# Performance work log

Hardware: AMD Instinct MI355X
Metric: run time of the kernel (lower is better)

Reference implementation:

```python
import jax, jax.numpy as jnp
import numpy as np

B, S, D, H, HD = 2, 2048, 1024, 16, 64
DFF = 4 * D
EPS = 1e-6


def _rms(x, w):
    return w * (x * jax.lax.rsqrt(jnp.mean(x * x, axis=-1, keepdims=True) + EPS))


def _rope(x, rope):
    # x: [B, H, S, HD], rope: [S, HD, 2]
    cos = rope[..., 0][None, None]
    sin = rope[..., 1][None, None]
    xr = x.reshape(*x.shape[:-1], -1, 2)
    rot = jnp.stack([-xr[..., 1], xr[..., 0]], axis=-1).reshape(x.shape)
    return x * cos + rot * sin


def setup_inputs() -> dict:
    key = jax.random.key(0)
    ks = jax.random.split(key, 10)
    w = lambda k, shape: jax.random.normal(k, shape, jnp.float32) * 0.02
    return {
        "hidden_states": jax.random.normal(ks[0], (B, S, D), jnp.float32),
        "timestep": jax.random.normal(ks[1], (B, D), jnp.float32),
        "rope_pos_embed": jax.random.normal(ks[2], (S, HD, 2), jnp.float32),
        "adaln_w": w(ks[3], (6 * D, D)),
        "adaln_b": jnp.zeros((6 * D,), jnp.float32),
        "wq": w(ks[4], (D, D)),
        "wk": w(ks[5], (D, D)),
        "wv": w(ks[6], (D, D)),
        "wo": w(ks[7], (D, D)),
        "q_norm_w": jnp.ones((D,), jnp.float32),
        "k_norm_w": jnp.ones((D,), jnp.float32),
        "norm3_w": jnp.ones((D,), jnp.float32),
        "fc1_w": w(ks[8], (DFF, D)),
        "fc1_b": jnp.zeros((DFF,), jnp.float32),
        "fc2_w": w(ks[9], (D, DFF)),
        "fc2_b": jnp.zeros((D,), jnp.float32),
    }


def reference(hidden_states, timestep, rope_pos_embed, adaln_w, adaln_b,
              wq, wk, wv, wo, q_norm_w, k_norm_w, norm3_w,
              fc1_w, fc1_b, fc2_w, fc2_b):
    x = hidden_states  # [B, S, D]
    # AdaLayerNorm: emb = Linear(SiLU(timestep)) -> 6 modulation chunks, broadcast over seq
    emb = jax.nn.silu(timestep) @ adaln_w.T + adaln_b  # [B, 6D]
    sh_msa, sc_msa, g_msa, sh_mlp, sc_mlp, g_mlp = jnp.split(emb[:, None, :], 6, axis=-1)
    mu = jnp.mean(x, axis=-1, keepdims=True)
    var = jnp.mean((x - mu) ** 2, axis=-1, keepdims=True)
    ln = (x - mu) * jax.lax.rsqrt(var + EPS)
    xm = ln * (1.0 + sc_msa) + sh_msa  # modulated input to attention

    # Attention: projections + RMSNorm over inner_dim + RoPE + SDPA
    q = _rms(xm @ wq.T, q_norm_w)
    k = _rms(xm @ wk.T, k_norm_w)
    v = xm @ wv.T
    q = q.reshape(B, S, H, HD).transpose(0, 2, 1, 3)
    k = k.reshape(B, S, H, HD).transpose(0, 2, 1, 3)
    v = v.reshape(B, S, H, HD).transpose(0, 2, 1, 3)
    q = _rope(q, rope_pos_embed)
    k = _rope(k, rope_pos_embed)
    scores = jnp.einsum('bhqd,bhkd->bhqk', q, k) * (HD ** -0.5)
    attn = jax.nn.softmax(scores, axis=-1)
    o = jnp.einsum('bhqk,bhkd->bhqd', attn, v)
    o = o.transpose(0, 2, 1, 3).reshape(B, S, H * HD) @ wo.T

    h = x + g_msa * o  # gated residual

    # MLP branch with AdaLN scale/shift on RMSNorm output
    n3 = _rms(h, norm3_w)
    nm = n3 * (1.0 + sc_mlp) + sh_mlp
    ff = jax.nn.gelu(nm @ fc1_w.T + fc1_b, approximate=True) @ fc2_w.T + fc2_b
    return h + g_mlp * ff
```

## Files before the change

### kernel.cpp

```cpp
#include <hip/hip_runtime.h>
#include <cstdint>
#include <cstddef>

typedef unsigned short ushort_t;
typedef __attribute__((ext_vector_type(8))) short s8v;
typedef __attribute__((ext_vector_type(4))) short s4v;
typedef __attribute__((ext_vector_type(4))) float f4v;

#define MFMA16(a, b, c) __builtin_amdgcn_mfma_f32_16x16x32_bf16(a, b, c, 0, 0, 0)

__device__ __forceinline__ ushort_t f2bf(float f) {
  union { float f; unsigned u; } a; a.f = f;
  return (ushort_t)((a.u + 0x7fffu + ((a.u >> 16) & 1u)) >> 16);
}
__device__ __forceinline__ float bf2f(ushort_t h) {
  union { unsigned u; float f; } a; a.u = ((unsigned)h) << 16; return a.f;
}

__device__ __forceinline__ void gload16(const void* g, void* l) {
  __builtin_amdgcn_global_load_lds(
      (__attribute__((address_space(1))) void*)(uintptr_t)g,
      (__attribute__((address_space(3))) void*)(unsigned)(uintptr_t)l,
      16, 0, 0);
}

__launch_bounds__(256)
__global__ void convert_w(const float* __restrict__ wq, const float* __restrict__ wk,
                          const float* __restrict__ wv, const float* __restrict__ wo,
                          const float* __restrict__ f1, const float* __restrict__ f2,
                          ushort_t* __restrict__ dqkv, ushort_t* __restrict__ dwo,
                          ushort_t* __restrict__ df1, ushort_t* __restrict__ df2)
{
  const int blk = blockIdx.x;
  const float* src; ushort_t* dst; int off;
  if      (blk < 1024) { src = wq; dst = dqkv;            off = blk; }
  else if (blk < 2048) { src = wk; dst = dqkv + 1048576;  off = blk - 1024; }
  else if (blk < 3072) { src = wv; dst = dqkv + 2097152;  off = blk - 2048; }
  else if (blk < 4096) { src = wo; dst = dwo;             off = blk - 3072; }
  else if (blk < 8192) { src = f1; dst = df1;             off = blk - 4096; }
  else                 { src = f2; dst = df2;             off = blk - 8192; }
  const int idx = off * 1024 + threadIdx.x * 4;
  float4 v = *(const float4*)(src + idx);
  s4v o;
  o[0] = (short)f2bf(v.x); o[1] = (short)f2bf(v.y);
  o[2] = (short)f2bf(v.z); o[3] = (short)f2bf(v.w);
  *(s4v*)(dst + idx) = o;
}

__launch_bounds__(256)
__global__ void adaln(const float* __restrict__ ts, const float* __restrict__ w,
                      const float* __restrict__ bias, float* __restrict__ emb)
{
  const int j = blockIdx.x * 4 + (threadIdx.x >> 6);
  const int lane = threadIdx.x & 63;
  const float* wr = w + (size_t)j * 1024;
  float s0 = 0.f, s1 = 0.f;
  for (int i = lane; i < 1024; i += 64) {
    const float wv = wr[i];
    const float t0 = ts[i], t1 = ts[1024 + i];
    s0 += wv * (t0 / (1.f + __expf(-t0)));
    s1 += wv * (t1 / (1.f + __expf(-t1)));
  }
  #pragma unroll
  for (int m = 32; m; m >>= 1) { s0 += __shfl_down(s0, m); s1 += __shfl_down(s1, m); }
  if (!lane) { emb[j] = s0 + bias[j]; emb[6144 + j] = s1 + bias[j]; }
}

__launch_bounds__(256)
__global__ void ln_mod(const float* __restrict__ x, const float* __restrict__ emb,
                       ushort_t* __restrict__ xm)
{
  const int row = blockIdx.x, b = row >> 11, tid = threadIdx.x;
  const float* xr = x + (size_t)row * 1024;
  const int c = tid * 4;
  float4 v = *(const float4*)(xr + c);
  float s  = v.x + v.y + v.z + v.w;
  float s2 = v.x*v.x + v.y*v.y + v.z*v.z + v.w*v.w;
  #pragma unroll
  for (int m = 32; m; m >>= 1) { s += __shfl_down(s, m); s2 += __shfl_down(s2, m); }
  __shared__ float red[8];
  const int wave = tid >> 6, lane = tid & 63;
  if (!lane) { red[wave] = s; red[4 + wave] = s2; }
  __syncthreads();
  const float mu = (red[0] + red[1] + red[2] + red[3]) * (1.f / 1024.f);
  const float ms = (red[4] + red[5] + red[6] + red[7]) * (1.f / 1024.f);
  const float rstd = rsqrtf(ms - mu * mu + 1e-6f);
  const float* sh = emb + b * 6144;
  const float* sc = emb + b * 6144 + 1024;
  float4 shv = *(const float4*)(sh + c);
  float4 scv = *(const float4*)(sc + c);
  s4v ov;
  ov[0] = (short)f2bf((v.x - mu) * rstd * (1.f + scv.x) + shv.x);
  ov[1] = (short)f2bf((v.y - mu) * rstd * (1.f + scv.y) + shv.y);
  ov[2] = (short)f2bf((v.z - mu) * rstd * (1.f + scv.z) + shv.z);
  ov[3] = (short)f2bf((v.w - mu) * rstd * (1.f + scv.w) + shv.w);
  *(s4v*)(xm + (size_t)row * 1024 + c) = ov;
}

template<int EPI, int TN>
__launch_bounds__(256)
__global__ void gemm_bt(const ushort_t* __restrict__ A, const ushort_t* __restrict__ Bw,
                        int K, int N,
                        ushort_t* __restrict__ outb, float* __restrict__ outf,
                        const float* __restrict__ bias, const float* __restrict__ resid,
                        const float* __restrict__ emb, int gate_off)
{
  constexpr int JN = TN / 32;
  constexpr int BUFB = TN * 32;
  __shared__ ushort_t As[2 * 128 * 32];
  __shared__ ushort_t Bs[2 * BUFB];
  const int tid = threadIdx.x;
  const int wave = tid >> 6, lane = tid & 63;
  const int quad = lane >> 4, r = lane & 15;
  const int m0 = blockIdx.y * 128, n0 = blockIdx.x * TN;
  const int wm = (wave >> 1) * 64, wn = (wave & 1) * (TN / 2);

  const int srow = wave * 16 + (lane >> 2);
  const int scol = (lane & 3) * 8;
  const ushort_t* ag = A  + (size_t)(m0 + srow) * K + scol;
  const ushort_t* bg = Bw + (size_t)(n0 + srow) * K + scol;
  const size_t rowK64 = (size_t)64 * K;

  f4v acc[4][JN] = {};

  {
    ushort_t* as = As + wave * 512;
    ushort_t* bs = Bs + wave * 512;
    gload16(ag,          as);
    gload16(ag + rowK64, as + 2048);
    gload16(bg,          bs);
    if (TN == 128) gload16(bg + rowK64, bs + 2048);
    ag += 32; bg += 32;
  }

  const int nIter = K >> 5;
  int cur = 0;
  for (int it = 0; it < nIter - 1; it++) {
    __syncthreads();
    {
      ushort_t* as = As + (cur ^ 1) * 4096 + wave * 512;
      ushort_t* bs = Bs + (cur ^ 1) * BUFB + wave * 512;
      gload16(ag,          as);
      gload16(ag + rowK64, as + 2048);
      gload16(bg,          bs);
      if (TN == 128) gload16(bg + rowK64, bs + 2048);
      ag += 32; bg += 32;
    }
    const ushort_t* ab = As + cur * 4096;
    const ushort_t* bb = Bs + cur * BUFB;
    s8v af[4], bf[JN];
    #pragma unroll
    for (int i = 0; i < 4; i++)
      af[i] = *(const s8v*)(ab + (wm + i * 16 + r) * 32 + quad * 8);
    #pragma unroll
    for (int j = 0; j < JN; j++)
      bf[j] = *(const s8v*)(bb + (wn + j * 16 + r) * 32 + quad * 8);
    #pragma unroll
    for (int i = 0; i < 4; i++)
      #pragma unroll
      for (int j = 0; j < JN; j++)
        acc[i][j] = MFMA16(af[i], bf[j], acc[i][j]);
    cur ^= 1;
  }
  __syncthreads();
  {
    const ushort_t* ab = As + cur * 4096;
    const ushort_t* bb = Bs + cur * BUFB;
    s8v af[4], bf[JN];
    #pragma unroll
    for (int i = 0; i < 4; i++)
      af[i] = *(const s8v*)(ab + (wm + i * 16 + r) * 32 + quad * 8);
    #pragma unroll
    for (int j = 0; j < JN; j++)
      bf[j] = *(const s8v*)(bb + (wn + j * 16 + r) * 32 + quad * 8);
    #pragma unroll
    for (int i = 0; i < 4; i++)
      #pragma unroll
      for (int j = 0; j < JN; j++)
        acc[i][j] = MFMA16(af[i], bf[j], acc[i][j]);
  }

  #pragma unroll
  for (int i = 0; i < 4; i++) {
    const int row = m0 + wm + i * 16 + quad * 4;
    #pragma unroll
    for (int j = 0; j < JN; j++) {
      const int col = n0 + wn + j * 16 + r;
      #pragma unroll
      for (int rr = 0; rr < 4; rr++) {
        float v = acc[i][j][rr];
        const int rw = row + rr;
        const size_t idx = (size_t)rw * N + col;
        if (EPI == 0) {
          outb[idx] = f2bf(v);
        } else if (EPI == 1) {
          const int b = rw >> 11;
          outf[idx] = resid[idx] + emb[b * 6144 + gate_off + col] * v;
        } else if (EPI == 2) {
          v += bias[col];
          const float u = 0.7978845608028654f * (v + 0.044715f * v * v * v);
          const float e = __expf(2.f * u);
          const float th = 1.f - 2.f / (e + 1.f);
          outb[idx] = f2bf(0.5f * v * (1.f + th));
        } else {
          const int b = rw >> 11;
          outf[idx] = resid[idx] + emb[b * 6144 + gate_off + col] * (v + bias[col]);
        }
      }
    }
  }
}

__launch_bounds__(256)
__global__ void qkv_post(const ushort_t* __restrict__ qkv, const float* __restrict__ rope,
                         const float* __restrict__ qw, const float* __restrict__ kw,
                         ushort_t* __restrict__ q_r, ushort_t* __restrict__ k_r,
                         ushort_t* __restrict__ v_r)
{
  const int row = blockIdx.x, b = row >> 11, s = row & 2047, tid = threadIdx.x;
  const ushort_t* base = qkv + (size_t)row * 3072;
  const int c = tid * 4;
  s4v qv = *(const s4v*)(base + c);
  s4v kv = *(const s4v*)(base + 1024 + c);
  s4v vv = *(const s4v*)(base + 2048 + c);
  float qf[4], kf[4]; float sq = 0.f, sk = 0.f;
  #pragma unroll
  for (int i = 0; i < 4; i++) {
    qf[i] = bf2f((ushort_t)qv[i]); kf[i] = bf2f((ushort_t)kv[i]);
    sq += qf[i] * qf[i]; sk += kf[i] * kf[i];
  }
  #pragma unroll
  for (int m = 32; m; m >>= 1) { sq += __shfl_down(sq, m); sk += __shfl_down(sk, m); }
  __shared__ float red[8];
  const int wave = tid >> 6, lane = tid & 63;
  if (!lane) { red[wave] = sq; red[4 + wave] = sk; }
  __syncthreads();
  const float rq = rsqrtf((red[0]+red[1]+red[2]+red[3]) * (1.f/1024.f) + 1e-6f)
                   * 0.18033688011112042f;
  const float rk = rsqrtf((red[4]+red[5]+red[6]+red[7]) * (1.f/1024.f) + 1e-6f);

  const int h = c >> 6, d = c & 63;
  const float* rp = rope + ((size_t)s * 64 + d) * 2;
  float4 r01 = *(const float4*)(rp);
  float4 r23 = *(const float4*)(rp + 4);
  const float q0 = qf[0]*rq*qw[c], q1 = qf[1]*rq*qw[c+1];
  const float q2 = qf[2]*rq*qw[c+2], q3 = qf[3]*rq*qw[c+3];
  const float k0 = kf[0]*rk*kw[c], k1 = kf[1]*rk*kw[c+1];
  const float k2 = kf[2]*rk*kw[c+2], k3 = kf[3]*rk*kw[c+3];
  s4v qo, ko;
  qo[0] = (short)f2bf(q0 * r01.x - q1 * r01.y);
  qo[1] = (short)f2bf(q1 * r01.z + q0 * r01.w);
  qo[2] = (short)f2bf(q2 * r23.x - q3 * r23.y);
  qo[3] = (short)f2bf(q3 * r23.z + q2 * r23.w);
  ko[0] = (short)f2bf(k0 * r01.x - k1 * r01.y);
  ko[1] = (short)f2bf(k1 * r01.z + k0 * r01.w);
  ko[2] = (short)f2bf(k2 * r23.x - k3 * r23.y);
  ko[3] = (short)f2bf(k3 * r23.z + k2 * r23.w);
  const size_t rowbase = ((size_t)(b * 16 + h) * 2048 + s) * 64;
  const int d_s = (((d >> 3) ^ (s & 7)) << 3) | (d & 7);
  *(s4v*)(q_r + rowbase + d) = qo;
  *(s4v*)(k_r + rowbase + d_s) = ko;
  *(s4v*)(v_r + rowbase + d) = vv;
}

__launch_bounds__(256)
__global__ void vtrans(const ushort_t* __restrict__ v_r, ushort_t* __restrict__ v_t)
{
  const int bh = blockIdx.x >> 5, st = blockIdx.x & 31;
  const int s0 = st * 64;
  __shared__ ushort_t tile[64 * 72];
  const int tid = threadIdx.x;
  #pragma unroll
  for (int rep = 0; rep < 2; rep++) {
    const int idx = rep * 256 + tid;
    const int sr = idx >> 3, dc = (idx & 7) << 3;
    s8v val = *(const s8v*)(v_r + ((size_t)bh * 2048 + s0 + sr) * 64 + dc);
    *(s8v*)(tile + sr * 72 + dc) = val;
  }
  __syncthreads();
  #pragma unroll
  for (int rep = 0; rep < 2; rep++) {
    const int idx = rep * 256 + tid;
    const int d = idx >> 3;
    const int scs = (((idx & 7) ^ (d & 7)) << 3);
    s8v val;
    const int sc = (idx & 7) << 3;
    #pragma unroll
    for (int j = 0; j < 8; j++) val[j] = (short)tile[(sc + j) * 72 + d];
    *(s8v*)(v_t + ((size_t)bh * 64 + d) * 2048 + s0 + scs) = val;
  }
}

__launch_bounds__(256)
__global__ void flash(const ushort_t* __restrict__ q_r, const ushort_t* __restrict__ k_r,
                      const ushort_t* __restrict__ v_t, ushort_t* __restrict__ attn)
{
  __shared__ ushort_t Ksh[64 * 64];
  __shared__ ushort_t Vsh[64 * 64];
  __shared__ ushort_t Psh[4][16 * 64];
  const int bh = blockIdx.x >> 5, qb = blockIdx.x & 31;
  const int tid = threadIdx.x, wave = tid >> 6, lane = tid & 63;
  const int quad = lane >> 4, r = lane & 15;
  const int rx = r & 7;
  const int q0 = qb * 64 + wave * 16;
  const size_t bhS = (size_t)bh * 2048;

  s8v aq0 = *(const s8v*)(q_r + (bhS + q0 + r) * 64 + quad * 8);
  s8v aq1 = *(const s8v*)(q_r + (bhS + q0 + r) * 64 + 32 + quad * 8);

  f4v o[4] = {};
  float mi = -1e30f, li = 0.f;

  const ushort_t* kg = k_r + bhS * 64 + wave * 1024 + lane * 8;
  const ushort_t* vg0 = v_t + ((size_t)bh * 64 + wave * 16 + (lane >> 3)) * 2048
                        + (lane & 7) * 8;
  const ushort_t* vg1 = vg0 + (size_t)8 * 2048;
  ushort_t* kl0 = Ksh + wave * 1024;
  ushort_t* kl1 = Ksh + wave * 1024 + 512;
  ushort_t* vl0 = Vsh + wave * 1024;
  ushort_t* vl1 = Vsh + wave * 1024 + 512;
  ushort_t* pw = &Psh[wave][0];

  for (int kb = 0; kb < 2048; kb += 64) {
    __syncthreads();
    gload16(kg,        kl0);
    gload16(kg + 512,  kl1);
    gload16(vg0 + kb,  vl0);
    gload16(vg1 + kb,  vl1);
    kg += 64 * 64;
    __syncthreads();

    f4v st[4];
    #pragma unroll
    for (int t = 0; t < 4; t++) {
      const ushort_t* krow = Ksh + (t * 16 + r) * 64;
      s8v k0 = *(const s8v*)(krow + (((quad) ^ rx) << 3));
      s8v k1 = *(const s8v*)(krow + (((4 + quad) ^ rx) << 3));
      f4v z = {};
      z = MFMA16(k0, aq0, z);
      z = MFMA16(k1, aq1, z);
      st[t] = z;
    }

    float mloc = st[0][0];
    #pragma unroll
    for (int t = 0; t < 4; t++)
      #pragma unroll
      for (int rr = 0; rr < 4; rr++) mloc = fmaxf(mloc, st[t][rr]);
    mloc = fmaxf(mloc, __shfl_xor(mloc, 16));
    mloc = fmaxf(mloc, __shfl_xor(mloc, 32));
    const float mn = fmaxf(mi, mloc);
    const float al = exp2f(mi - mn);
    float ls = 0.f;
    float p[4][4];
    #pragma unroll
    for (int t = 0; t < 4; t++)
      #pragma unroll
      for (int rr = 0; rr < 4; rr++) {
        p[t][rr] = exp2f(st[t][rr] - mn);
        ls += p[t][rr];
      }
    ls += __shfl_xor(ls, 16);
    ls += __shfl_xor(ls, 32);
    li = al * li + ls;
    mi = mn;

    #pragma unroll
    for (int t = 0; t < 4; t++) {
      s4v pb;
      pb[0] = (short)f2bf(p[t][0]); pb[1] = (short)f2bf(p[t][1]);
      pb[2] = (short)f2bf(p[t][2]); pb[3] = (short)f2bf(p[t][3]);
      const int idx = r * 64 + (((((t << 1) | (quad >> 1))) ^ rx) << 3) + (quad & 1) * 4;
      *(s4v*)(pw + idx) = pb;
    }

    float alo[4];
    #pragma unroll
    for (int rr = 0; rr < 4; rr++) alo[rr] = __shfl(al, quad * 4 + rr);
    #pragma unroll
    for (int nt = 0; nt < 4; nt++)
      #pragma unroll
      for (int rr = 0; rr < 4; rr++) o[nt][rr] *= alo[rr];

    asm volatile("s_waitcnt lgkmcnt(0)" ::: "memory");

    #pragma unroll
    for (int kc = 0; kc < 2; kc++) {
      s8v ap = *(const s8v*)(pw + r * 64 + ((((kc << 2) | quad) ^ rx) << 3));
      #pragma unroll
      for (int nt = 0; nt < 4; nt++) {
        s8v bv = *(const s8v*)(Vsh + (nt * 16 + r) * 64 + ((((kc << 2) | quad) ^ rx) << 3));
        o[nt] = MFMA16(ap, bv, o[nt]);
      }
    }
  }

  const int h = bh & 15, b = bh >> 4;
  const float linv = 1.f / li;
  #pragma unroll
  for (int rr = 0; rr < 4; rr++) {
    const float inv = __shfl(linv, quad * 4 + rr);
    const size_t orow = ((size_t)(b * 2048 + q0 + quad * 4 + rr)) * 1024 + h * 64;
    #pragma unroll
    for (int nt = 0; nt < 4; nt++)
      attn[orow + nt * 16 + r] = f2bf(o[nt][rr] * inv);
  }
}

__launch_bounds__(256)
__global__ void rms3_mod(const float* __restrict__ h, const float* __restrict__ emb,
                         const float* __restrict__ w3, ushort_t* __restrict__ nm)
{
  const int row = blockIdx.x, b = row >> 11, tid = threadIdx.x;
  const float* hr = h + (size_t)row * 1024;
  const int c = tid * 4;
  float4 v = *(const float4*)(hr + c);
  float s2 = v.x*v.x + v.y*v.y + v.z*v.z + v.w*v.w;
  #pragma unroll
  for (int m = 32; m; m >>= 1) s2 += __shfl_down(s2, m);
  __shared__ float red[4];
  const int wave = tid >> 6, lane = tid & 63;
  if (!lane) red[wave] = s2;
  __syncthreads();
  const float rms = rsqrtf((red[0] + red[1] + red[2] + red[3]) * (1.f / 1024.f) + 1e-6f);
  const float* sh = emb + b * 6144 + 3072;
  const float* sc = emb + b * 6144 + 4096;
  float4 shv = *(const float4*)(sh + c);
  float4 scv = *(const float4*)(sc + c);
  float4 wv  = *(const float4*)(w3 + c);
  s4v ov;
  ov[0] = (short)f2bf(v.x * rms * wv.x * (1.f + scv.x) + shv.x);
  ov[1] = (short)f2bf(v.y * rms * wv.y * (1.f + scv.y) + shv.y);
  ov[2] = (short)f2bf(v.z * rms * wv.z * (1.f + scv.z) + shv.z);
  ov[3] = (short)f2bf(v.w * rms * wv.w * (1.f + scv.w) + shv.w);
  *(s4v*)(nm + (size_t)row * 1024 + c) = ov;
}

extern "C" void kernel_launch(void* const* d_in, const int* in_sizes, int n_in,
                              void* d_out, int out_size, void* d_ws, size_t ws_size,
                              hipStream_t stream)
{
  const float* x    = (const float*)d_in[0];
  const float* ts   = (const float*)d_in[1];
  const float* rope = (const float*)d_in[2];
  const float* adw  = (const float*)d_in[3];
  const float* adb  = (const float*)d_in[4];
  const float* wq   = (const float*)d_in[5];
  const float* wk   = (const float*)d_in[6];
  const float* wv   = (const float*)d_in[7];
  const float* wo   = (const float*)d_in[8];
  const float* qnw  = (const float*)d_in[9];
  const float* knw  = (const float*)d_in[10];
  const float* n3w  = (const float*)d_in[11];
  const float* f1w  = (const float*)d_in[12];
  const float* f1b  = (const float*)d_in[13];
  const float* f2w  = (const float*)d_in[14];
  const float* f2b  = (const float*)d_in[15];

  char* ws = (char*)d_ws;
  ushort_t* WQKV = (ushort_t*)(ws + 0);
  ushort_t* WO   = (ushort_t*)(ws + 6291456);
  ushort_t* F1   = (ushort_t*)(ws + 8388608);
  ushort_t* F2   = (ushort_t*)(ws + 16777216);
  float*    EMB  = (float*)   (ws + 25165824);
  float*    H    = (float*)   (ws + 25214976);
  ushort_t* XM   = (ushort_t*)(ws + 41992192);
  ushort_t* QKV  = (ushort_t*)(ws + 50380800);
  ushort_t* QR   = (ushort_t*)(ws + 75546624);
  ushort_t* KR   = (ushort_t*)(ws + 83935232);
  ushort_t* VR   = (ushort_t*)(ws + 92323840);
  ushort_t* VT   = (ushort_t*)(ws + 100712448);
  ushort_t* ATTN = XM;
  ushort_t* NM   = QKV;
  ushort_t* FF1  = QR;

  convert_w<<<12288, 256, 0, stream>>>(wq, wk, wv, wo, f1w, f2w, WQKV, WO, F1, F2);
  adaln<<<1536, 256, 0, stream>>>(ts, adw, adb, EMB);
  ln_mod<<<4096, 256, 0, stream>>>(x, EMB, XM);
  gemm_bt<0, 128><<<dim3(24, 32), 256, 0, stream>>>(XM, WQKV, 1024, 3072,
      QKV, nullptr, nullptr, nullptr, nullptr, 0);
  qkv_post<<<4096, 256, 0, stream>>>(QKV, rope, qnw, knw, QR, KR, VR);
  vtrans<<<1024, 256, 0, stream>>>(VR, VT);
  flash<<<1024, 256, 0, stream>>>(QR, KR, VT, ATTN);
  gemm_bt<1, 64><<<dim3(16, 32), 256, 0, stream>>>(ATTN, WO, 1024, 1024,
      nullptr, H, nullptr, x, EMB, 2048);
  rms3_mod<<<4096, 256, 0, stream>>>(H, EMB, n3w, NM);
  gemm_bt<2, 128><<<dim3(32, 32), 256, 0, stream>>>(NM, F1, 1024, 4096,
      FF1, nullptr, f1b, nullptr, nullptr, 0);
  gemm_bt<3, 64><<<dim3(16, 32), 256, 0, stream>>>(FF1, F2, 4096, 1024,
      nullptr, (float*)d_out, f2b, H, EMB, 5120);
}
```

Before: 441.9 us.

## Double flash attention KV tile to 128 and use fast exp2 and packed bf16 rounding

The flash kernel now processes 128 keys per iteration instead of 64, which halves the number of barrier pairs and online-softmax rescales per key. It also swaps exp2f for the hardware exp2 builtin and packs bf16 P values with a simple rounding add plus byte-perm instead of round-to-nearest-even. The trade-off is double the shared memory and more registers per wave (eight score tiles), which can lower occupancy. The bf16 rounding changes slightly from ties-to-even to round-half-up.

```diff
diff --git a/kernel.cpp b/kernel.cpp
--- a/kernel.cpp
+++ b/kernel.cpp
@@ -15,6 +15,9 @@
 }
 __device__ __forceinline__ float bf2f(ushort_t h) {
   union { unsigned u; float f; } a; a.u = ((unsigned)h) << 16; return a.f;
+}
+__device__ __forceinline__ unsigned fbits(float f) {
+  union { float f; unsigned u; } a; a.f = f; return a.u;
 }
 
 __device__ __forceinline__ void gload16(const void* g, void* l) {
@@ -295,9 +298,9 @@
 __global__ void flash(const ushort_t* __restrict__ q_r, const ushort_t* __restrict__ k_r,
                       const ushort_t* __restrict__ v_t, ushort_t* __restrict__ attn)
 {
-  __shared__ ushort_t Ksh[64 * 64];
-  __shared__ ushort_t Vsh[64 * 64];
-  __shared__ ushort_t Psh[4][16 * 64];
+  __shared__ ushort_t Ksh[128 * 64];
+  __shared__ ushort_t Vsh[64 * 128];
+  __shared__ ushort_t Psh[4][16 * 128];
   const int bh = blockIdx.x >> 5, qb = blockIdx.x & 31;
   const int tid = threadIdx.x, wave = tid >> 6, lane = tid & 63;
   const int quad = lane >> 4, r = lane & 15;
@@ -311,30 +314,27 @@
   f4v o[4] = {};
   float mi = -1e30f, li = 0.f;
 
-  const ushort_t* kg = k_r + bhS * 64 + wave * 1024 + lane * 8;
-  const ushort_t* vg0 = v_t + ((size_t)bh * 64 + wave * 16 + (lane >> 3)) * 2048
-                        + (lane & 7) * 8;
-  const ushort_t* vg1 = vg0 + (size_t)8 * 2048;
-  ushort_t* kl0 = Ksh + wave * 1024;
-  ushort_t* kl1 = Ksh + wave * 1024 + 512;
-  ushort_t* vl0 = Vsh + wave * 1024;
-  ushort_t* vl1 = Vsh + wave * 1024 + 512;
+  const ushort_t* kg = k_r + (bhS + wave * 32 + (lane >> 3)) * 64 + (lane & 7) * 8;
+  ushort_t* kl = Ksh + wave * 2048 + lane * 8;
+  const ushort_t* vg = v_t + ((size_t)bh * 64 + wave * 16 + (lane >> 4)) * 2048
+                       + (lane & 15) * 8;
+  ushort_t* vl = Vsh + (wave * 16 + (lane >> 4)) * 128 + (lane & 15) * 8;
   ushort_t* pw = &Psh[wave][0];
 
-  for (int kb = 0; kb < 2048; kb += 64) {
+  for (int kb = 0; kb < 2048; kb += 128) {
     __syncthreads();
-    gload16(kg,        kl0);
-    gload16(kg + 512,  kl1);
-    gload16(vg0 + kb,  vl0);
-    gload16(vg1 + kb,  vl1);
-    kg += 64 * 64;
+    #pragma unroll
+    for (int c = 0; c < 4; c++) {
+      gload16(kg + (size_t)(kb + c * 8) * 64, kl + c * 512);
+      gload16(vg + kb + (size_t)(c * 4) * 2048, vl + c * 512);
+    }
     __syncthreads();
 
-    f4v st[4];
-    #pragma unroll
-    for (int t = 0; t < 4; t++) {
+    f4v st[8];
+    #pragma unroll
+    for (int t = 0; t < 8; t++) {
       const ushort_t* krow = Ksh + (t * 16 + r) * 64;
-      s8v k0 = *(const s8v*)(krow + (((quad) ^ rx) << 3));
+      s8v k0 = *(const s8v*)(krow + ((quad ^ rx) << 3));
       s8v k1 = *(const s8v*)(krow + (((4 + quad) ^ rx) << 3));
       f4v z = {};
       z = MFMA16(k0, aq0, z);
@@ -344,20 +344,20 @@
 
     float mloc = st[0][0];
     #pragma unroll
-    for (int t = 0; t < 4; t++)
+    for (int t = 0; t < 8; t++)
       #pragma unroll
       for (int rr = 0; rr < 4; rr++) mloc = fmaxf(mloc, st[t][rr]);
     mloc = fmaxf(mloc, __shfl_xor(mloc, 16));
     mloc = fmaxf(mloc, __shfl_xor(mloc, 32));
     const float mn = fmaxf(mi, mloc);
-    const float al = exp2f(mi - mn);
+    const float al = __builtin_amdgcn_exp2f(mi - mn);
+    float p[8][4];
     float ls = 0.f;
-    float p[4][4];
-    #pragma unroll
-    for (int t = 0; t < 4; t++)
+    #pragma unroll
+    for (int t = 0; t < 8; t++)
       #pragma unroll
       for (int rr = 0; rr < 4; rr++) {
-        p[t][rr] = exp2f(st[t][rr] - mn);
+        p[t][rr] = __builtin_amdgcn_exp2f(st[t][rr] - mn);
         ls += p[t][rr];
       }
     ls += __shfl_xor(ls, 16);
@@ -366,12 +366,17 @@
     mi = mn;
 
     #pragma unroll
-    for (int t = 0; t < 4; t++) {
-      s4v pb;
-      pb[0] = (short)f2bf(p[t][0]); pb[1] = (short)f2bf(p[t][1]);
-      pb[2] = (short)f2bf(p[t][2]); pb[3] = (short)f2bf(p[t][3]);
-      const int idx = r * 64 + (((((t << 1) | (quad >> 1))) ^ rx) << 3) + (quad & 1) * 4;
-      *(s4v*)(pw + idx) = pb;
+    for (int t = 0; t < 8; t++) {
+      const unsigned u0 = fbits(p[t][0]) + 0x8000u;
+      const unsigned u1 = fbits(p[t][1]) + 0x8000u;
+      const unsigned u2 = fbits(p[t][2]) + 0x8000u;
+      const unsigned u3 = fbits(p[t][3]) + 0x8000u;
+      uint2 pk;
+      pk.x = __builtin_amdgcn_perm(u1, u0, 0x07060302u);
+      pk.y = __builtin_amdgcn_perm(u3, u2, 0x07060302u);
+      const int cw = t * 2 + (quad >> 1);
+      const int sc = (cw & 8) | ((cw & 7) ^ rx);
+      *(uint2*)(pw + r * 128 + (sc << 3) + (quad & 1) * 4) = pk;
     }
 
     float alo[4];
@@ -385,11 +390,13 @@
     asm volatile("s_waitcnt lgkmcnt(0)" ::: "memory");
 
     #pragma unroll
-    for (int kc = 0; kc < 2; kc++) {
-      s8v ap = *(const s8v*)(pw + r * 64 + ((((kc << 2) | quad) ^ rx) << 3));
+    for (int kc = 0; kc < 4; kc++) {
+      const int c = kc * 4 + quad;
+      const int sc = (c & 8) | ((c & 7) ^ rx);
+      s8v ap = *(const s8v*)(pw + r * 128 + (sc << 3));
       #pragma unroll
       for (int nt = 0; nt < 4; nt++) {
-        s8v bv = *(const s8v*)(Vsh + (nt * 16 + r) * 64 + ((((kc << 2) | quad) ^ rx) << 3));
+        s8v bv = *(const s8v*)(Vsh + (nt * 16 + r) * 128 + (sc << 3));
         o[nt] = MFMA16(ap, bv, o[nt]);
       }
     }
```

Result: no change. 434.4 us (-1.7%).
